# Kernel optimization log

Hardware: AMD Instinct MI355X
Metric: run time of the kernel (lower is better)

## Reference

```python
import jax, jax.numpy as jnp
import numpy as np

B, S, H, NH = 2, 2048, 4096, 32
HD = H // NH
EPS = 1e-8


def setup_inputs() -> dict:
    key = jax.random.key(0)
    ks = jax.random.split(key, 6)
    return {
        "hidden_states": jax.random.normal(ks[0], (B, S, H), jnp.float32),
        "residual": jax.random.normal(ks[1], (B, S, H), jnp.float32),
        # BLOOM alibi: [batch*num_heads, 1, kv_len]
        "alibi": jax.random.normal(ks[2], (B * NH, 1, S), jnp.float32) * 0.1,
        "attention_mask": jnp.ones((B, S), jnp.bool_),  # unused by this forward path
        "W_qkv": jax.random.normal(ks[3], (3 * H, H), jnp.float32) * (1.0 / np.sqrt(H)),
        "b_qkv": jnp.zeros((3 * H,), jnp.float32),
        "W_dense": jax.random.normal(ks[4], (H, H), jnp.float32) * (1.0 / np.sqrt(H)),
        "b_dense": jnp.zeros((H,), jnp.float32),
    }


def reference(hidden_states, residual, alibi, attention_mask, W_qkv, b_qkv, W_dense, b_dense):
    b, s, h = hidden_states.shape
    nh, hd = NH, h // NH
    inv_norm_factor = 1.0 / np.sqrt(hd)  # attention.inv_norm_factor
    beta = 1.0                            # attention.beta (BLOOM default)

    # fused qkv projection + BLOOM _split_heads: [b, s, nh, 3, hd]
    fused = hidden_states @ W_qkv.T + b_qkv
    fused = fused.reshape(b, s, nh, 3, hd)
    q, k, v = fused[..., 0, :], fused[..., 1, :], fused[..., 2, :]  # each [b, s, nh, hd]
    # The torch permute/reshape round-trips leave reshaped_{q,k,v} = [b, s, nh, hd].

    # offset_key = inv_norm_factor * k + beta * (pinv(Q) * alibi) permuted back
    q_bnsd = jnp.transpose(q, (0, 2, 1, 3))           # [b, nh, s, hd]
    pinv_q = jnp.linalg.pinv(q_bnsd)                   # [b, nh, hd, s]
    alibi4 = alibi.reshape(b, nh, 1, s)                # broadcast over hd
    bias = jnp.transpose(pinv_q * alibi4, (0, 3, 1, 2))  # [b, s, nh, hd]
    offset_k = inv_norm_factor * k + beta * bias

    # memory_efficient_attention on [b, s, nh, hd]: einsum 'b h i d, b h j d' ->
    # attention ACROSS HEADS per sequence position; no mask, no causal, no dropout.
    # Chunked online softmax == single stable softmax with +eps in denominator.
    scale = hd ** -0.5  # q additionally scaled inside memory_efficient_attention
    w = jnp.einsum('bsid,bsjd->bsij', q * scale, offset_k)  # [b, s, nh, nh]
    m = jax.lax.stop_gradient(jnp.max(w, axis=-1, keepdims=True))
    e = jnp.exp(w - m)
    ctx = jnp.einsum('bsij,bsjd->bsid', e, v) / (jnp.sum(e, axis=-1, keepdims=True) + EPS)

    ctx = ctx.reshape(b, s, h)  # flatten(start_dim=2)
    out = ctx @ W_dense.T + b_dense + residual  # dense + dropout_add (eval: p=0)
    return out
```

## Files before the change

kernel.cpp:

```cpp
#include <hip/hip_runtime.h>

#define B_  2
#define S_  2048
#define NH_ 32
#define HD_ 128
#define H_  4096
#define H3_ 12288
#define GP_ 8

typedef __bf16 bf16x8 __attribute__((ext_vector_type(8)));
typedef float  f32x4  __attribute__((ext_vector_type(4)));

__device__ __forceinline__ unsigned short f2bf(float f) {
  unsigned int u = __float_as_uint(f);
  u += 0x7fffu + ((u >> 16) & 1u);
  return (unsigned short)(u >> 16);
}
__device__ __forceinline__ void unpack8(uint4 r, float f[8]) {
  f[0] = __uint_as_float(r.x << 16); f[1] = __uint_as_float(r.x & 0xffff0000u);
  f[2] = __uint_as_float(r.y << 16); f[3] = __uint_as_float(r.y & 0xffff0000u);
  f[4] = __uint_as_float(r.z << 16); f[5] = __uint_as_float(r.z & 0xffff0000u);
  f[6] = __uint_as_float(r.w << 16); f[7] = __uint_as_float(r.w & 0xffff0000u);
}
__device__ __forceinline__ void gload_lds16(const void* g, void* l) {
  __builtin_amdgcn_global_load_lds(
      (const __attribute__((address_space(1))) unsigned int*)g,
      (__attribute__((address_space(3))) unsigned int*)l, 16, 0, 0);
}

__global__ __launch_bounds__(256) void cvt_bf16(const float* __restrict__ in,
                                                unsigned short* __restrict__ out,
                                                long n) {
  long i = ((long)blockIdx.x * 256 + threadIdx.x) * 4;
  const long stride = (long)gridDim.x * 256 * 4;
  for (; i < n; i += stride) {
    float4 v = *(const float4*)(in + i);
    ushort4 o;
    o.x = f2bf(v.x); o.y = f2bf(v.y); o.z = f2bf(v.z); o.w = f2bf(v.w);
    *(ushort4*)(out + i) = o;
  }
}

template <int EPI>
__global__ __launch_bounds__(512, 2) void gemm256(
    const unsigned short* __restrict__ A, const unsigned short* __restrict__ Bt,
    void* __restrict__ C, const float* __restrict__ bias, const float* __restrict__ Res,
    int lda, int ldb, int ldc, int K)
{
  __shared__ __align__(16) unsigned short lds[3 * 16384];

  const int tid = threadIdx.x;
  const int w = tid >> 6, l = tid & 63;

  const int gx = gridDim.x;
  const int nwg = gx * gridDim.y;
  const int flat = blockIdx.y * gx + blockIdx.x;
  const int swz = (flat & 7) * (nwg >> 3) + (flat >> 3);
  const int m0 = (swz / gx) * 256;
  const int n0 = (swz % gx) * 256;

  const int wr = w >> 2, wc = w & 3;
  const int lr16 = l & 15, kq = l >> 4;

  const int srow = w * 16 + (l >> 2);
  const int scs  = (((l & 3) ^ ((l >> 3) & 3)) << 3);
  const unsigned short* ga = A  + (long)(m0 + srow) * lda + scs;
  const unsigned short* gb = Bt + (long)(n0 + srow) * ldb + scs;
  unsigned short* sb_w = lds + w * 512;

  const int rchunk = ((kq ^ ((l >> 1) & 3)) << 3);

  const int NT = K >> 5;

  const f32x4 zero = {0.f, 0.f, 0.f, 0.f};
  f32x4 acc[8][4];
#pragma unroll
  for (int m = 0; m < 8; ++m)
#pragma unroll
    for (int n = 0; n < 4; ++n) acc[m][n] = zero;

  auto stage = [&](int kt, int s) {
    const unsigned short* a = ga + (long)kt * 32;
    const unsigned short* b = gb + (long)kt * 32;
    unsigned short* d = sb_w + s * 16384;
    gload_lds16(a,                  d);
    gload_lds16(a + 128L * lda,     d + 4096);
    gload_lds16(b,                  d + 8192);
    gload_lds16(b + 128L * ldb,     d + 12288);
  };

  stage(0, 0);
  stage(1, 1);
  asm volatile("s_waitcnt vmcnt(4)" ::: "memory");
  __builtin_amdgcn_s_barrier();

  for (int t = 0; t < NT; ++t) {
    const int cur = t % 3;
    if (t + 2 < NT) stage(t + 2, (t + 2) % 3);

    const unsigned short* sa = lds + cur * 16384;
    const unsigned short* sbB = sa + 8192;
    bf16x8 av[8], bv[4];
#pragma unroll
    for (int n = 0; n < 4; ++n)
      bv[n] = *(const bf16x8*)&sbB[(wc * 64 + n * 16 + lr16) * 32 + rchunk];
#pragma unroll
    for (int m = 0; m < 8; ++m)
      av[m] = *(const bf16x8*)&sa[(wr * 128 + m * 16 + lr16) * 32 + rchunk];

    __builtin_amdgcn_s_setprio(1);
#pragma unroll
    for (int m = 0; m < 8; ++m)
#pragma unroll
      for (int n = 0; n < 4; ++n)
        acc[m][n] = __builtin_amdgcn_mfma_f32_16x16x32_bf16(av[m], bv[n], acc[m][n], 0, 0, 0);
    __builtin_amdgcn_s_setprio(0);

    if (t + 1 < NT) {
      if (t + 2 < NT) asm volatile("s_waitcnt vmcnt(4)" ::: "memory");
      else            asm volatile("s_waitcnt vmcnt(0)" ::: "memory");
      __builtin_amdgcn_s_barrier();
    }
  }

#pragma unroll
  for (int m = 0; m < 8; ++m) {
    const int grow0 = m0 + wr * 128 + m * 16 + kq * 4;
#pragma unroll
    for (int n = 0; n < 4; ++n) {
      const int gcol = n0 + wc * 64 + n * 16 + lr16;
#pragma unroll
      for (int i = 0; i < 4; ++i) {
        const long gi = (long)(grow0 + i) * ldc + gcol;
        float v = acc[m][n][i];
        if (EPI == 0) {
          ((unsigned short*)C)[gi] = f2bf(v + bias[gcol]);
        } else {
          ((float*)C)[gi] = v + bias[gcol] + Res[gi];
        }
      }
    }
  }
}

template <int EPI>
__global__ __launch_bounds__(256) void gemm_bt(
    const unsigned short* __restrict__ Abase, const unsigned short* __restrict__ Bbase,
    void* __restrict__ Cbase, const float* __restrict__ bias, const float* __restrict__ Res,
    int lda, int ldb, int ldc, int K,
    long sAb, long sAn, long sBb, long sBn, long sCb, long sCn)
{
  __shared__ __align__(16) unsigned short As[128][32];
  __shared__ __align__(16) unsigned short Bs[128][32];

  const int zz = blockIdx.z;
  const int zb = zz >> 5, zn = zz & 31;
  const unsigned short* A  = Abase + (long)zb * sAb + (long)zn * sAn;
  const unsigned short* Bm = Bbase + (long)zb * sBb + (long)zn * sBn;
  const long coff = (long)zb * sCb + (long)zn * sCn;

  const int m0 = blockIdx.y * 128;
  const int n0 = blockIdx.x * 128;
  const int tid = threadIdx.x;
  const int wave = tid >> 6;
  const int lane = tid & 63;
  const int wr = wave >> 1, wc = wave & 1;
  const int lr = lane & 15, kq = lane >> 4;
  const int srow = wave * 16 + (lane >> 2);
  const int scol = (((lane & 3) ^ ((lane >> 3) & 3)) << 3);
  const int rch  = ((kq ^ ((lane >> 1) & 3)) << 3);

  const f32x4 zero = {0.0f, 0.0f, 0.0f, 0.0f};
  f32x4 acc[4][4];
#pragma unroll
  for (int m = 0; m < 4; ++m)
#pragma unroll
    for (int n = 0; n < 4; ++n) acc[m][n] = zero;

  for (int k0 = 0; k0 < K; k0 += 32) {
    const unsigned short* ga = A  + (long)(m0 + srow) * lda + k0 + scol;
    const unsigned short* gb = Bm + (long)(n0 + srow) * ldb + k0 + scol;
    gload_lds16(ga,                   &As[wave * 16][0]);
    gload_lds16(ga + (long)64 * lda,  &As[64 + wave * 16][0]);
    gload_lds16(gb,                   &Bs[wave * 16][0]);
    gload_lds16(gb + (long)64 * ldb,  &Bs[64 + wave * 16][0]);
    __syncthreads();

    bf16x8 av[4], bv[4];
#pragma unroll
    for (int m = 0; m < 4; ++m) av[m] = *(const bf16x8*)&As[wr * 64 + m * 16 + lr][rch];
#pragma unroll
    for (int n = 0; n < 4; ++n) bv[n] = *(const bf16x8*)&Bs[wc * 64 + n * 16 + lr][rch];
#pragma unroll
    for (int m = 0; m < 4; ++m)
#pragma unroll
      for (int n = 0; n < 4; ++n)
        acc[m][n] = __builtin_amdgcn_mfma_f32_16x16x32_bf16(av[m], bv[n], acc[m][n], 0, 0, 0);
    __syncthreads();
  }

#pragma unroll
  for (int m = 0; m < 4; ++m) {
    const int grow0 = m0 + wr * 64 + m * 16 + kq * 4;
#pragma unroll
    for (int n = 0; n < 4; ++n) {
      const int gcol = n0 + wc * 64 + n * 16 + lr;
#pragma unroll
      for (int r = 0; r < 4; ++r) {
        const long gi = coff + (long)(grow0 + r) * ldc + gcol;
        float v = acc[m][n][r];
        if (EPI == 0) {
          ((unsigned short*)Cbase)[gi] = f2bf(v + bias[gcol]);
        } else if (EPI == 1) {
          ((float*)Cbase)[gi] = v + bias[gcol] + Res[gi];
        } else {
          ((unsigned short*)Cbase)[gi] = f2bf(v);
        }
      }
    }
  }
}

__global__ __launch_bounds__(256) void compute_g(const unsigned short* __restrict__ fused,
                                                 float* __restrict__ Gpart)
{
  __shared__ float Qs[64][128];
  const int z = blockIdx.x;
  const int b = z >> 5, n = z & 31;
  const unsigned short* Q = fused + (long)b * S_ * H3_ + n * 384;
  const int t = threadIdx.x;
  const int t1 = t >> 4, t2 = t & 15;
  float acc[8][8];
#pragma unroll
  for (int a = 0; a < 8; ++a)
#pragma unroll
    for (int c = 0; c < 8; ++c) acc[a][c] = 0.f;

  const int sbeg = blockIdx.y * (S_ / GP_);
  for (int s0 = sbeg; s0 < sbeg + S_ / GP_; s0 += 64) {
#pragma unroll
    for (int ii = 0; ii < 4; ++ii) {
      const int r = ii * 16 + t1;
      float f[8];
      unpack8(*(const uint4*)(Q + (long)(s0 + r) * H3_ + t2 * 8), f);
#pragma unroll
      for (int j = 0; j < 8; ++j) Qs[r][t2 * 8 + j] = f[j];
    }
    __syncthreads();
    for (int ss = 0; ss < 64; ++ss) {
      float qa[8], qb[8];
#pragma unroll
      for (int j = 0; j < 8; ++j) { qa[j] = Qs[ss][t1 * 8 + j]; qb[j] = Qs[ss][t2 * 8 + j]; }
#pragma unroll
      for (int a = 0; a < 8; ++a)
#pragma unroll
        for (int c = 0; c < 8; ++c) acc[a][c] += qa[a] * qb[c];
    }
    __syncthreads();
  }
  float* Gp = Gpart + ((long)z * GP_ + blockIdx.y) * 16384;
#pragma unroll
  for (int a = 0; a < 8; ++a)
#pragma unroll
    for (int cc = 0; cc < 2; ++cc) {
      float4 v = make_float4(acc[a][cc * 4], acc[a][cc * 4 + 1],
                             acc[a][cc * 4 + 2], acc[a][cc * 4 + 3]);
      *(float4*)&Gp[(t1 * 8 + a) * 128 + t2 * 8 + cc * 4] = v;
    }
}

__global__ __launch_bounds__(1024) void invert_g(const float* __restrict__ Gpart,
                                                 unsigned short* __restrict__ Ginv)
{
  __shared__ __align__(16) float prow[2][128];
  __shared__ __align__(16) float pcol[2][128];
  const int z = blockIdx.x;
  const int t = threadIdx.x;
  const int c  = t & 127;
  const int rg = t >> 7;
  const float* Gz = Gpart + (long)z * GP_ * 16384;

  float a[16];
#pragma unroll
  for (int i = 0; i < 16; ++i) {
    const int idx = (rg * 16 + i) * 128 + c;
    float s = 0.f;
#pragma unroll
    for (int p = 0; p < GP_; ++p) s += Gz[p * 16384 + idx];
    a[i] = s;
  }

  for (int p = 0; p < 128; ++p) {
    const int buf = p & 1;
    const int prg = p >> 4, pi = p & 15;
    if (rg == prg) {
      float v = a[0];
#pragma unroll
      for (int i = 1; i < 16; ++i) v = (pi == i) ? a[i] : v;
      prow[buf][c] = v;
    }
    if (c == p) {
#pragma unroll
      for (int q = 0; q < 4; ++q) {
        float4 w4 = make_float4(a[q * 4], a[q * 4 + 1], a[q * 4 + 2], a[q * 4 + 3]);
        *(float4*)&pcol[buf][rg * 16 + q * 4] = w4;
      }
    }
    __syncthreads();
    const float invp = 1.0f / prow[buf][p];
    const float rowv = (c == p) ? invp : prow[buf][c] * invp;
#pragma unroll
    for (int q = 0; q < 4; ++q) {
      const float4 pc4 = *(const float4*)&pcol[buf][rg * 16 + q * 4];
      const float pcv[4] = {pc4.x, pc4.y, pc4.z, pc4.w};
#pragma unroll
      for (int j = 0; j < 4; ++j) {
        const int i = q * 4 + j;
        const int r = rg * 16 + i;
        const float cur = (c == p) ? 0.f : a[i];
        a[i] = (r == p) ? rowv : cur - pcv[j] * rowv;
      }
    }
  }
  unsigned short* Oz = Ginv + (long)z * 16384;
#pragma unroll
  for (int i = 0; i < 16; ++i) Oz[(rg * 16 + i) * 128 + c] = f2bf(a[i]);
}

__global__ __launch_bounds__(256) void attn_pos(
    const unsigned short* __restrict__ fused, const unsigned short* __restrict__ Zb,
    const float* __restrict__ alibi, unsigned short* __restrict__ ctx)
{
  __shared__ __align__(16) unsigned short qkv[H3_];
  __shared__ __align__(16) unsigned short zsh[H_];
  __shared__ float wsh[NH_][NH_ + 1];
  __shared__ float pden[NH_];
  __shared__ float alib[NH_];

  const int s = blockIdx.x, b = blockIdx.y;
  const int t = threadIdx.x;
  const unsigned short* src = fused + ((long)b * S_ + s) * H3_;
  for (int i = t * 8; i < H3_; i += 2048) *(uint4*)&qkv[i] = *(const uint4*)&src[i];
  const unsigned short* zsrc = Zb + ((long)b * S_ + s) * H_;
  for (int i = t * 8; i < H_; i += 2048) *(uint4*)&zsh[i] = *(const uint4*)&zsrc[i];
  if (t < NH_) alib[t] = 0.08838834764831845f * alibi[((long)(b * NH_ + t)) * S_ + s];
  __syncthreads();

  const int i = t >> 3;
  const int j0 = (t & 7) * 4;
  const int rot = (i ^ (t & 7)) & 15;
  float aqk[4] = {0.f, 0.f, 0.f, 0.f};
  float aqz[4] = {0.f, 0.f, 0.f, 0.f};
  for (int dbi = 0; dbi < 16; ++dbi) {
    const int d0b = ((dbi + rot) & 15) * 8;
    float qf[8];
    unpack8(*(const uint4*)&qkv[i * 384 + d0b], qf);
#pragma unroll
    for (int jj = 0; jj < 4; ++jj) {
      const int j = j0 + jj;
      float kf[8], zf[8];
      unpack8(*(const uint4*)&qkv[j * 384 + 128 + d0b], kf);
      unpack8(*(const uint4*)&zsh[j * 128 + d0b], zf);
#pragma unroll
      for (int d = 0; d < 8; ++d) { aqk[jj] += qf[d] * kf[d]; aqz[jj] += qf[d] * zf[d]; }
    }
  }
  float wv[4];
#pragma unroll
  for (int jj = 0; jj < 4; ++jj)
    wv[jj] = 0.0078125f * aqk[jj] + alib[j0 + jj] * aqz[jj];
  float vmax = fmaxf(fmaxf(wv[0], wv[1]), fmaxf(wv[2], wv[3]));
  vmax = fmaxf(vmax, __shfl_xor(vmax, 1));
  vmax = fmaxf(vmax, __shfl_xor(vmax, 2));
  vmax = fmaxf(vmax, __shfl_xor(vmax, 4));
  float ssum = 0.f;
#pragma unroll
  for (int jj = 0; jj < 4; ++jj) { wv[jj] = __expf(wv[jj] - vmax); ssum += wv[jj]; }
#pragma unroll
  for (int jj = 0; jj < 4; ++jj) wsh[i][j0 + jj] = wv[jj];
  ssum += __shfl_xor(ssum, 1);
  ssum += __shfl_xor(ssum, 2);
  ssum += __shfl_xor(ssum, 4);
  if ((t & 7) == 0) pden[i] = 1.0f / (ssum + 1e-8f);
  __syncthreads();

  const int d0 = (t & 7) * 16;
  float acc[16];
#pragma unroll
  for (int d = 0; d < 16; ++d) acc[d] = 0.f;
  for (int j = 0; j < NH_; ++j) {
    const float p = wsh[i][j];
    float vf[16];
    unpack8(*(const uint4*)&qkv[j * 384 + 256 + d0], vf);
    unpack8(*(const uint4*)&qkv[j * 384 + 256 + d0 + 8], vf + 8);
#pragma unroll
    for (int d = 0; d < 16; ++d) acc[d] += p * vf[d];
  }
  const float inv = pden[i];
  union { uint4 u[2]; unsigned short us[16]; } ov;
#pragma unroll
  for (int d = 0; d < 16; ++d) ov.us[d] = f2bf(acc[d] * inv);
  unsigned short* cp = ctx + ((long)b * S_ + s) * H_ + i * HD_ + d0;
  *(uint4*)&cp[0] = ov.u[0];
  *(uint4*)&cp[8] = ov.u[1];
}

extern "C" void kernel_launch(void* const* d_in, const int* in_sizes, int n_in,
                              void* d_out, int out_size, void* d_ws, size_t ws_size,
                              hipStream_t stream)
{
  (void)in_sizes; (void)n_in; (void)out_size; (void)ws_size;
  const float* hidden   = (const float*)d_in[0];
  const float* residual = (const float*)d_in[1];
  const float* alibi    = (const float*)d_in[2];
  const float* Wqkv     = (const float*)d_in[4];
  const float* bqkv     = (const float*)d_in[5];
  const float* Wd       = (const float*)d_in[6];
  const float* bd       = (const float*)d_in[7];
  float* out = (float*)d_out;

  char* ws = (char*)d_ws;
  size_t off = 0;
  auto carve = [&](size_t bytes) -> void* {
    void* p = ws + off;
    off += (bytes + 255) & ~(size_t)255;
    return p;
  };
  const long nHid = (long)B_ * S_ * H_;
  const long nWq  = (long)H3_ * H_;
  unsigned short* hid_bf   = (unsigned short*)carve((size_t)nHid * 2);
  unsigned short* wqkv_bf  = (unsigned short*)carve((size_t)nWq * 2);
  unsigned short* wd_bf    = (unsigned short*)carve((size_t)H_ * H_ * 2);
  unsigned short* fused_bf = (unsigned short*)carve((size_t)B_ * S_ * H3_ * 2);
  unsigned short* z_bf     = (unsigned short*)carve((size_t)nHid * 2);
  unsigned short* ctx_bf   = (unsigned short*)carve((size_t)nHid * 2);
  float*          Gpart    = (float*)carve((size_t)64 * GP_ * 16384 * 4);
  unsigned short* ginv_bf  = (unsigned short*)carve((size_t)64 * 16384 * 2);

  cvt_bf16<<<2048, 256, 0, stream>>>(hidden, hid_bf, nHid);
  cvt_bf16<<<2048, 256, 0, stream>>>(Wqkv, wqkv_bf, nWq);
  cvt_bf16<<<2048, 256, 0, stream>>>(Wd, wd_bf, (long)H_ * H_);

  gemm256<0><<<dim3(H3_ / 256, (B_ * S_) / 256, 1), 512, 0, stream>>>(
      hid_bf, wqkv_bf, fused_bf, bqkv, nullptr, H_, H_, H3_, H_);

  compute_g<<<dim3(64, GP_), 256, 0, stream>>>(fused_bf, Gpart);
  invert_g<<<64, 1024, 0, stream>>>(Gpart, ginv_bf);

  gemm_bt<2><<<dim3(1, S_ / 128, 64), 256, 0, stream>>>(
      fused_bf, ginv_bf, z_bf, nullptr, nullptr, H3_, HD_, H_, HD_,
      (long)S_ * H3_, 384, (long)32 * 16384, 16384, (long)S_ * H_, HD_);

  attn_pos<<<dim3(S_, B_), 256, 0, stream>>>(fused_bf, z_bf, alibi, ctx_bf);

  gemm256<1><<<dim3(H_ / 256, (B_ * S_) / 256, 1), 512, 0, stream>>>(
      ctx_bf, wd_bf, out, bd, residual, H_, H_, H_, H_);
}
```

Baseline: 864.2 us.

## Compute Gram matrix with bf16 MFMA and fuse three conversion kernels

Rewrites compute_g so Q^T Q per head is computed with 32x32x16 bf16 MFMA instructions from a padded bf16 LDS tile, replacing the scalar fp32 outer-product loop. It also merges the three fp32-to-bf16 conversion launches into one kernel to cut launch overhead. Accumulation stays fp32 but the LDS reads are scalar 16-bit gathers, which may limit throughput.

```diff
diff --git a/kernel.cpp b/kernel.cpp
--- a/kernel.cpp
+++ b/kernel.cpp
@@ -10,6 +10,7 @@
 
 typedef __bf16 bf16x8 __attribute__((ext_vector_type(8)));
 typedef float  f32x4  __attribute__((ext_vector_type(4)));
+typedef float  f32x16 __attribute__((ext_vector_type(16)));
 
 __device__ __forceinline__ unsigned short f2bf(float f) {
   unsigned int u = __float_as_uint(f);
@@ -28,17 +29,25 @@
       (__attribute__((address_space(3))) unsigned int*)l, 16, 0, 0);
 }
 
-__global__ __launch_bounds__(256) void cvt_bf16(const float* __restrict__ in,
-                                                unsigned short* __restrict__ out,
-                                                long n) {
-  long i = ((long)blockIdx.x * 256 + threadIdx.x) * 4;
-  const long stride = (long)gridDim.x * 256 * 4;
-  for (; i < n; i += stride) {
+__device__ __forceinline__ void cvt_seg(const float* __restrict__ in,
+                                        unsigned short* __restrict__ out,
+                                        long n, long base, long stride) {
+  for (long i = base; i < n; i += stride) {
     float4 v = *(const float4*)(in + i);
     ushort4 o;
     o.x = f2bf(v.x); o.y = f2bf(v.y); o.z = f2bf(v.z); o.w = f2bf(v.w);
     *(ushort4*)(out + i) = o;
   }
+}
+__global__ __launch_bounds__(256) void cvt3(
+    const float* __restrict__ a, unsigned short* __restrict__ oa, long na,
+    const float* __restrict__ b, unsigned short* __restrict__ ob, long nb,
+    const float* __restrict__ c, unsigned short* __restrict__ oc, long nc) {
+  const long base = ((long)blockIdx.x * 256 + threadIdx.x) * 4;
+  const long stride = (long)gridDim.x * 256 * 4;
+  cvt_seg(a, oa, na, base, stride);
+  cvt_seg(b, ob, nb, base, stride);
+  cvt_seg(c, oc, nc, base, stride);
 }
 
 template <int EPI>
@@ -224,49 +233,76 @@
 __global__ __launch_bounds__(256) void compute_g(const unsigned short* __restrict__ fused,
                                                  float* __restrict__ Gpart)
 {
-  __shared__ float Qs[64][128];
+  __shared__ __align__(16) unsigned short Qs[64 * 136];
   const int z = blockIdx.x;
   const int b = z >> 5, n = z & 31;
   const unsigned short* Q = fused + (long)b * S_ * H3_ + n * 384;
   const int t = threadIdx.x;
-  const int t1 = t >> 4, t2 = t & 15;
-  float acc[8][8];
-#pragma unroll
-  for (int a = 0; a < 8; ++a)
-#pragma unroll
-    for (int c = 0; c < 8; ++c) acc[a][c] = 0.f;
+  const int w = t >> 6, l = t & 63;
+  const int l31 = l & 31, hi = l >> 5;
+  const int ar0 = (w & 1) * 2, ac0 = (w >> 1) * 2;
+
+  f32x16 acc[2][2];
+#pragma unroll
+  for (int i = 0; i < 2; ++i)
+#pragma unroll
+    for (int j = 0; j < 2; ++j)
+#pragma unroll
+      for (int r = 0; r < 16; ++r) acc[i][j][r] = 0.f;
 
   const int sbeg = blockIdx.y * (S_ / GP_);
-  for (int s0 = sbeg; s0 < sbeg + S_ / GP_; s0 += 64) {
-#pragma unroll
-    for (int ii = 0; ii < 4; ++ii) {
-      const int r = ii * 16 + t1;
-      float f[8];
-      unpack8(*(const uint4*)(Q + (long)(s0 + r) * H3_ + t2 * 8), f);
-#pragma unroll
-      for (int j = 0; j < 8; ++j) Qs[r][t2 * 8 + j] = f[j];
-    }
+
+  for (int ss0 = 0; ss0 < S_ / GP_; ss0 += 64) {
     __syncthreads();
-    for (int ss = 0; ss < 64; ++ss) {
-      float qa[8], qb[8];
-#pragma unroll
-      for (int j = 0; j < 8; ++j) { qa[j] = Qs[ss][t1 * 8 + j]; qb[j] = Qs[ss][t2 * 8 + j]; }
-#pragma unroll
-      for (int a = 0; a < 8; ++a)
-#pragma unroll
-        for (int c = 0; c < 8; ++c) acc[a][c] += qa[a] * qb[c];
+#pragma unroll
+    for (int pass = 0; pass < 4; ++pass) {
+      const int sL = pass * 16 + (t >> 4);
+      const int c = t & 15;
+      uint4 v = *(const uint4*)(Q + (long)(sbeg + ss0 + sL) * H3_ + c * 8);
+      *(uint4*)&Qs[sL * 136 + c * 8] = v;
     }
     __syncthreads();
-  }
+
+#pragma unroll
+    for (int ks = 0; ks < 4; ++ks) {
+      const int sb = ks * 16 + hi * 8;
+      bf16x8 fa[2], fb[2];
+#pragma unroll
+      for (int i = 0; i < 2; ++i) {
+        const int colA = (ar0 + i) * 32 + l31;
+        const int colB = (ac0 + i) * 32 + l31;
+        bf16x8 ra, rbv;
+#pragma unroll
+        for (int j = 0; j < 8; ++j) {
+          unsigned short ua = Qs[(sb + j) * 136 + colA];
+          unsigned short ub = Qs[(sb + j) * 136 + colB];
+          ra[j]  = *reinterpret_cast<__bf16*>(&ua);
+          rbv[j] = *reinterpret_cast<__bf16*>(&ub);
+        }
+        fa[i] = ra; fb[i] = rbv;
+      }
+#pragma unroll
+      for (int i = 0; i < 2; ++i)
+#pragma unroll
+        for (int j = 0; j < 2; ++j)
+          acc[i][j] = __builtin_amdgcn_mfma_f32_32x32x16_bf16(fa[i], fb[j], acc[i][j], 0, 0, 0);
+    }
+  }
+
   float* Gp = Gpart + ((long)z * GP_ + blockIdx.y) * 16384;
 #pragma unroll
-  for (int a = 0; a < 8; ++a)
-#pragma unroll
-    for (int cc = 0; cc < 2; ++cc) {
-      float4 v = make_float4(acc[a][cc * 4], acc[a][cc * 4 + 1],
-                             acc[a][cc * 4 + 2], acc[a][cc * 4 + 3]);
-      *(float4*)&Gp[(t1 * 8 + a) * 128 + t2 * 8 + cc * 4] = v;
-    }
+  for (int i = 0; i < 2; ++i) {
+    const int rowb = (ar0 + i) * 32 + 4 * hi;
+#pragma unroll
+    for (int j = 0; j < 2; ++j) {
+      const int col = (ac0 + j) * 32 + l31;
+#pragma unroll
+      for (int r = 0; r < 16; ++r) {
+        const int row = rowb + (r & 3) + 8 * (r >> 2);
+        Gp[row * 128 + col] = acc[i][j][r];
+      }
+    }
+  }
 }
 
 __global__ __launch_bounds__(1024) void invert_g(const float* __restrict__ Gpart,
@@ -437,9 +473,9 @@
   float*          Gpart    = (float*)carve((size_t)64 * GP_ * 16384 * 4);
   unsigned short* ginv_bf  = (unsigned short*)carve((size_t)64 * 16384 * 2);
 
-  cvt_bf16<<<2048, 256, 0, stream>>>(hidden, hid_bf, nHid);
-  cvt_bf16<<<2048, 256, 0, stream>>>(Wqkv, wqkv_bf, nWq);
-  cvt_bf16<<<2048, 256, 0, stream>>>(Wd, wd_bf, (long)H_ * H_);
+  cvt3<<<2048, 256, 0, stream>>>(hidden, hid_bf, nHid,
+                                 Wqkv, wqkv_bf, nWq,
+                                 Wd, wd_bf, (long)H_ * H_);
 
   gemm256<0><<<dim3(H3_ / 256, (B_ * S_) / 256, 1), 512, 0, stream>>>(
       hid_bf, wqkv_bf, fused_bf, bqkv, nullptr, H_, H_, H3_, H_);
```

New measurement: 822.9 us. 1.05x faster.
